# Performance work log

Measured on AMD Instinct MI355X. Metric: run time of the kernel, lower is better.

Reference implementation:

```python
import jax, jax.numpy as jnp
import numpy as np

GROUPS = 8
EPS = 1e-3  # keras GroupNormalization default epsilon


def group_norm(x, gamma, beta):
    # Keras GroupNormalization(axis=-1): reduce over all non-batch, non-group axes.
    B, L, C = x.shape
    xg = x.reshape(B, L, GROUPS, C // GROUPS)
    mean = jnp.mean(xg, axis=(1, 3), keepdims=True)          # [B,1,G,1]
    var = jnp.var(xg, axis=(1, 3), keepdims=True)
    xn = ((xg - mean) * jax.lax.rsqrt(var + EPS)).reshape(B, L, C)
    return xn * gamma + beta


def setup_inputs() -> dict:
    key = jax.random.key(0)
    ks = jax.random.split(key, 6)
    B, L, C = 8, 2048, 512
    x = jax.random.normal(ks[0], (B, L, C), dtype=jnp.float32)
    s = 0.02
    return {
        "x": x,
        "gamma": jnp.ones((C,), jnp.float32),
        "beta": jnp.zeros((C,), jnp.float32),
        "wq": jax.random.normal(ks[1], (C, C), jnp.float32) * s,
        "bq": jnp.zeros((C,), jnp.float32),
        "wk": jax.random.normal(ks[2], (C, C), jnp.float32) * s,
        "bk": jnp.zeros((C,), jnp.float32),
        "wv": jax.random.normal(ks[3], (C, C), jnp.float32) * s,
        "bv": jnp.zeros((C,), jnp.float32),
        "wp": jax.random.normal(ks[4], (C, C), jnp.float32) * s,
        "bp": jnp.zeros((C,), jnp.float32),
    }


def reference(x, gamma, beta, wq, bq, wk, bk, wv, bv, wp, bp):
    C = x.shape[-1]
    scale = jnp.float32(C) ** -0.5
    h = group_norm(x, gamma, beta)                           # normalized input (also residual!)
    q = h @ wq + bq                                          # [B,L,C]
    k = h @ wk + bk
    v = h @ wv + bv
    attn = jnp.einsum('blc,bLc->blL', q, k) * scale          # [B,L,L]
    attn = jax.nn.softmax(attn, axis=-1)
    o = jnp.einsum('blL,bLc->blc', attn, v)                  # [B,L,C]
    o = o @ wp + bp
    return h + o
```

## Files before the change

kernel.cpp:

```cpp
#include <hip/hip_runtime.h>
#include <hip/hip_bf16.h>
#include <cstdint>

typedef unsigned short ushort_t;
typedef __bf16  bf16x8 __attribute__((ext_vector_type(8)));
typedef float   f32x4  __attribute__((ext_vector_type(4)));

#define L_SEQ 2048
#define C_DIM 512
#define B_SZ  8
#define N_GROUPS 8
#define CG 64

__device__ __forceinline__ float bf2f(ushort_t u) {
    union { uint32_t i; float f; } x; x.i = ((uint32_t)u) << 16; return x.f;
}
__device__ __forceinline__ ushort_t f2bf(float f) {
    union { float f; uint32_t i; } x; x.f = f;
    uint32_t i = x.i;
    uint32_t r = (i + 0x7FFFu + ((i >> 16) & 1u)) >> 16;
    return (ushort_t)r;
}

__device__ __forceinline__ void gl_lds16(const ushort_t* g, ushort_t* l) {
    __builtin_amdgcn_global_load_lds(
        (const __attribute__((address_space(1))) unsigned int*)g,
        (__attribute__((address_space(3))) unsigned int*)l, 16, 0, 0);
}

__global__ __launch_bounds__(256) void conv_wT(const float* __restrict__ wq,
                                               const float* __restrict__ wk,
                                               const float* __restrict__ wv,
                                               const float* __restrict__ wp,
                                               ushort_t* __restrict__ wqkvT,
                                               ushort_t* __restrict__ wpT) {
    __shared__ ushort_t Ts[64][72];
    int blk = blockIdx.x, tid = threadIdx.x;
    int mat = blk >> 6, t = blk & 63;
    int k0 = (t >> 3) * 64, n0 = (t & 7) * 64;
    const float* srcs[4] = {wq, wk, wv, wp};
    const float* src = srcs[mat];
    #pragma unroll
    for (int i = 0; i < 2; ++i) {
        int idx = tid * 2 + i;
        int row = idx >> 3, c8 = (idx & 7) * 8;
        const float* p = src + (size_t)(k0 + row) * 512 + n0 + c8;
        float4 a = *(const float4*)p;
        float4 b = *(const float4*)(p + 4);
        Ts[row][c8 + 0] = f2bf(a.x); Ts[row][c8 + 1] = f2bf(a.y);
        Ts[row][c8 + 2] = f2bf(a.z); Ts[row][c8 + 3] = f2bf(a.w);
        Ts[row][c8 + 4] = f2bf(b.x); Ts[row][c8 + 5] = f2bf(b.y);
        Ts[row][c8 + 6] = f2bf(b.z); Ts[row][c8 + 7] = f2bf(b.w);
    }
    __syncthreads();
    int dr = tid >> 2, lc = (tid & 3) * 16;
    union { uint4 v[2]; ushort_t u[16]; } o;
    #pragma unroll
    for (int j = 0; j < 16; ++j) o.u[j] = Ts[lc + j][dr];
    ushort_t* dst = (mat == 3 ? wpT + (size_t)(n0 + dr) * 512
                              : wqkvT + (size_t)(mat * 512 + n0 + dr) * 512) + k0 + lc;
    *(uint4*)dst = o.v[0];
    *(uint4*)(dst + 8) = o.v[1];
}

__global__ __launch_bounds__(256) void gn_stats(const float* __restrict__ x,
                                                float* __restrict__ sums) {
    int bg = blockIdx.x >> 3, sp = blockIdx.x & 7;
    int b = bg >> 3, g = bg & 7;
    int tid = threadIdx.x;
    const float* base = x + ((size_t)b * L_SEQ + sp * 256) * C_DIM + g * CG;
    float s = 0.f, s2 = 0.f;
    #pragma unroll
    for (int it = 0; it < 8; ++it) {
        int i = it * 2048 + tid * 8;
        int l = i >> 6, c = i & 63;
        const float* p = base + (size_t)l * C_DIM + c;
        float4 a = *(const float4*)p;
        float4 bb = *(const float4*)(p + 4);
        s  += a.x + a.y + a.z + a.w + bb.x + bb.y + bb.z + bb.w;
        s2 += a.x*a.x + a.y*a.y + a.z*a.z + a.w*a.w
            + bb.x*bb.x + bb.y*bb.y + bb.z*bb.z + bb.w*bb.w;
    }
    #pragma unroll
    for (int off = 32; off > 0; off >>= 1) { s += __shfl_down(s, off); s2 += __shfl_down(s2, off); }
    __shared__ float rs[4], rs2[4];
    int wave = tid >> 6;
    if ((tid & 63) == 0) { rs[wave] = s; rs2[wave] = s2; }
    __syncthreads();
    if (tid == 0) {
        sums[bg * 16 + sp * 2 + 0] = rs[0] + rs[1] + rs[2] + rs[3];
        sums[bg * 16 + sp * 2 + 1] = rs2[0] + rs2[1] + rs2[2] + rs2[3];
    }
}

__global__ __launch_bounds__(256) void gn_apply(const float* __restrict__ x,
                                                const float* __restrict__ gamma,
                                                const float* __restrict__ beta,
                                                const float* __restrict__ sums,
                                                ushort_t* __restrict__ h) {
    size_t e = ((size_t)blockIdx.x * 256 + threadIdx.x) * 8;
    int c = (int)(e % C_DIM);
    size_t bl = e / C_DIM;
    int b = (int)(bl / L_SEQ);
    int g = c >> 6;
    int bg = b * 8 + g;
    float s = 0.f, s2 = 0.f;
    #pragma unroll
    for (int sp = 0; sp < 8; ++sp) { s += sums[bg * 16 + sp * 2]; s2 += sums[bg * 16 + sp * 2 + 1]; }
    const float N = (float)(L_SEQ * CG);
    float mean = s / N;
    float var  = s2 / N - mean * mean;
    float rstd = rsqrtf(var + 1e-3f);
    float4 a = *(const float4*)(x + e);
    float4 bb = *(const float4*)(x + e + 4);
    float xf[8] = {a.x, a.y, a.z, a.w, bb.x, bb.y, bb.z, bb.w};
    union { uint4 v; ushort_t u[8]; } o;
    #pragma unroll
    for (int i = 0; i < 8; ++i)
        o.u[i] = f2bf((xf[i] - mean) * rstd * gamma[c + i] + beta[c + i]);
    *(uint4*)(h + e) = o.v;
}

template<int MODE>
__global__ __launch_bounds__(256) void gemm128(const ushort_t* __restrict__ A,
                                               const ushort_t* __restrict__ BT,
                                               const float* __restrict__ b0,
                                               const float* __restrict__ b1,
                                               const ushort_t* __restrict__ res,
                                               ushort_t* __restrict__ o0,
                                               ushort_t* __restrict__ o1,
                                               float* __restrict__ of) {
    __shared__ ushort_t As[128][64];
    __shared__ ushort_t Bs[128][64];
    int tid = threadIdx.x, lane = tid & 63, w = tid >> 6;
    int l15 = lane & 15, quad = lane >> 4;
    int m0 = blockIdx.y * 128;
    int n0g = blockIdx.x * 128;
    int wm = w >> 1, wn = w & 1;
    int lr8 = lane >> 3;
    int gch = (lane & 7) ^ lr8;
    int h8  = l15 & 7;
    f32x4 acc[4][4] = {};
    for (int k0 = 0; k0 < 512; k0 += 64) {
        #pragma unroll
        for (int j = 0; j < 4; ++j) {
            int rb = w * 32 + j * 8;
            int r  = rb + lr8;
            gl_lds16(A  + (size_t)(m0 + r) * 512 + k0 + gch * 8, &As[rb][0]);
            gl_lds16(BT + (size_t)(n0g + r) * 512 + k0 + gch * 8, &Bs[rb][0]);
        }
        __syncthreads();
        #pragma unroll
        for (int kk = 0; kk < 2; ++kk) {
            int slot = ((quad + 4 * kk) ^ h8) * 8;
            bf16x8 af[4], bf[4];
            #pragma unroll
            for (int t = 0; t < 4; ++t) {
                af[t] = *(const bf16x8*)&As[wm * 64 + t * 16 + l15][slot];
                bf[t] = *(const bf16x8*)&Bs[wn * 64 + t * 16 + l15][slot];
            }
            #pragma unroll
            for (int mt = 0; mt < 4; ++mt)
                #pragma unroll
                for (int nt = 0; nt < 4; ++nt)
                    acc[mt][nt] = __builtin_amdgcn_mfma_f32_16x16x32_bf16(af[mt], bf[nt], acc[mt][nt], 0, 0, 0);
        }
        __syncthreads();
    }
    #pragma unroll
    for (int mt = 0; mt < 4; ++mt)
        #pragma unroll
        for (int nt = 0; nt < 4; ++nt) {
            int n = (MODE == 0 ? (n0g & 511) : n0g) + wn * 64 + nt * 16 + l15;
            float bvn = (MODE == 2) ? 0.f : (MODE == 1 ? b0[n] : (n0g >> 9 ? b1[n] : b0[n]));
            #pragma unroll
            for (int r = 0; r < 4; ++r) {
                int m = m0 + wm * 64 + mt * 16 + quad * 4 + r;
                float v = acc[mt][nt][r];
                if (MODE == 2) {
                    v += b0[m];
                    o0[(size_t)(n >> 11) * 1048576 + (size_t)m * 2048 + (n & 2047)] = f2bf(v);
                } else if (MODE == 1) {
                    of[(size_t)m * 512 + n] = v + bvn + bf2f(res[(size_t)m * 512 + n]);
                } else {
                    ushort_t* ob = (n0g >> 9) ? o1 : o0;
                    ob[(size_t)m * 512 + n] = f2bf(v + bvn);
                }
            }
        }
}

__global__ __launch_bounds__(768, 3) void attn11(const ushort_t* __restrict__ Q,
                                                 const ushort_t* __restrict__ K,
                                                 const ushort_t* __restrict__ vT,
                                                 ushort_t* __restrict__ O) {
    __shared__ ushort_t Ks[2][32][520];
    __shared__ ushort_t Vs[2][512][32];
    __shared__ ushort_t Ps[2][64][40];
    __shared__ float    Al[2][64];
    __shared__ float    Lb[64];
    int tid = threadIdx.x;
    int lane = tid & 63, w = tid >> 6;
    int l15 = lane & 15, quad = lane >> 4;
    int b  = blockIdx.x & 7;
    int qt = blockIdx.x >> 3;
    const float scale2 = 0.044194173824159216f * 1.4426950408889634f;
    const ushort_t* Qb = Q + (size_t)b * L_SEQ * C_DIM;
    const ushort_t* Kb = K + (size_t)b * L_SEQ * C_DIM;
    const ushort_t* Vt = vT + (size_t)b * C_DIM * L_SEQ;
    ushort_t* Ob = O + (size_t)b * L_SEQ * C_DIM;

    bool isQK = (w < 4);
    int pw = w - 4;
    int d0 = pw * 64;

    bf16x8 qf[16];
    float m_r = -1e30f, l_r = 0.f;
    f32x4 acc[4][4];

    if (isQK) {
        int qr = qt * 64 + w * 16 + l15;
        #pragma unroll
        for (int ks = 0; ks < 16; ++ks)
            qf[ks] = *(const bf16x8*)(Qb + (size_t)qr * C_DIM + ks * 32 + quad * 8);
    } else {
        #pragma unroll
        for (int qi = 0; qi < 4; ++qi)
            #pragma unroll
            for (int nt = 0; nt < 4; ++nt) acc[qi][nt] = (f32x4){0.f, 0.f, 0.f, 0.f};
        #pragma unroll
        for (int i = 0; i < 4; ++i) {
            int row = pw * 4 + i;
            gl_lds16(Kb + (size_t)row * C_DIM + lane * 8, &Ks[0][row][0]);
        }
    }
    __syncthreads();

    for (int kt = 0; kt <= 64; ++kt) {
        int cur = kt & 1, prv = cur ^ 1;
        if (isQK) {
            if (kt < 64) {
                f32x4 s0a = (f32x4){0.f, 0.f, 0.f, 0.f};
                f32x4 s0b = (f32x4){0.f, 0.f, 0.f, 0.f};
                f32x4 s1a = (f32x4){0.f, 0.f, 0.f, 0.f};
                f32x4 s1b = (f32x4){0.f, 0.f, 0.f, 0.f};
                __builtin_amdgcn_s_setprio(1);
                #pragma unroll
                for (int ks = 0; ks < 16; ks += 2) {
                    bf16x8 kf0 = *(const bf16x8*)&Ks[cur][l15][ks * 32 + quad * 8];
                    bf16x8 kf1 = *(const bf16x8*)&Ks[cur][16 + l15][ks * 32 + quad * 8];
                    bf16x8 kf2 = *(const bf16x8*)&Ks[cur][l15][(ks + 1) * 32 + quad * 8];
                    bf16x8 kf3 = *(const bf16x8*)&Ks[cur][16 + l15][(ks + 1) * 32 + quad * 8];
                    s0a = __builtin_amdgcn_mfma_f32_16x16x32_bf16(kf0, qf[ks], s0a, 0, 0, 0);
                    s1a = __builtin_amdgcn_mfma_f32_16x16x32_bf16(kf1, qf[ks], s1a, 0, 0, 0);
                    s0b = __builtin_amdgcn_mfma_f32_16x16x32_bf16(kf2, qf[ks + 1], s0b, 0, 0, 0);
                    s1b = __builtin_amdgcn_mfma_f32_16x16x32_bf16(kf3, qf[ks + 1], s1b, 0, 0, 0);
                }
                __builtin_amdgcn_s_setprio(0);
                f32x4 s0 = s0a + s0b;
                f32x4 s1 = s1a + s1b;
                float mx = fmaxf(fmaxf(fmaxf(s0[0], s0[1]), fmaxf(s0[2], s0[3])),
                                 fmaxf(fmaxf(s1[0], s1[1]), fmaxf(s1[2], s1[3])));
                mx = fmaxf(mx, __shfl_xor(mx, 16, 64));
                mx = fmaxf(mx, __shfl_xor(mx, 32, 64));
                mx *= scale2;
                float mn = fmaxf(m_r, mx);
                float alpha = exp2f(m_r - mn);
                m_r = mn;
                ushort_t pb[8];
                float rs = 0.f;
                #pragma unroll
                for (int r = 0; r < 4; ++r) {
                    pb[r]     = f2bf(exp2f(s0[r] * scale2 - mn));
                    pb[4 + r] = f2bf(exp2f(s1[r] * scale2 - mn));
                    rs += bf2f(pb[r]) + bf2f(pb[4 + r]);
                }
                rs += __shfl_xor(rs, 16, 64);
                rs += __shfl_xor(rs, 32, 64);
                l_r = l_r * alpha + rs;
                int row = w * 16 + l15;
                uint2 w0, w1;
                w0.x = (uint32_t)pb[0] | ((uint32_t)pb[1] << 16);
                w0.y = (uint32_t)pb[2] | ((uint32_t)pb[3] << 16);
                w1.x = (uint32_t)pb[4] | ((uint32_t)pb[5] << 16);
                w1.y = (uint32_t)pb[6] | ((uint32_t)pb[7] << 16);
                *(uint2*)&Ps[cur][row][quad * 4] = w0;
                *(uint2*)&Ps[cur][row][16 + quad * 4] = w1;
                if (lane < 16) Al[cur][w * 16 + lane] = alpha;
            } else {
                if (lane < 16) Lb[w * 16 + lane] = l_r;
            }
        } else {
            if (kt < 63) {
                #pragma unroll
                for (int i = 0; i < 4; ++i) {
                    int row = pw * 4 + i;
                    gl_lds16(Kb + (size_t)((kt + 1) * 32 + row) * C_DIM + lane * 8, &Ks[prv][row][0]);
                }
            }
            if (kt < 64) {
                int k0 = kt * 32;
                #pragma unroll
                for (int i = 0; i < 4; ++i) {
                    int r0 = (pw * 4 + i) * 16;
                    gl_lds16(Vt + (size_t)(r0 + (lane >> 2)) * L_SEQ + k0 + (lane & 3) * 8,
                             &Vs[cur][r0][0]);
                }
            }
            if (kt > 0) {
                bf16x8 pf[4];
                #pragma unroll
                for (int qi = 0; qi < 4; ++qi)
                    pf[qi] = *(const bf16x8*)&Ps[prv][qi * 16 + l15][quad * 8];
                #pragma unroll
                for (int qi = 0; qi < 4; ++qi) {
                    float4 av = *(const float4*)&Al[prv][qi * 16 + quad * 4];
                    #pragma unroll
                    for (int nt = 0; nt < 4; ++nt) {
                        acc[qi][nt][0] *= av.x; acc[qi][nt][1] *= av.y;
                        acc[qi][nt][2] *= av.z; acc[qi][nt][3] *= av.w;
                    }
                }
                bf16x8 vf[4];
                #pragma unroll
                for (int nt = 0; nt < 4; ++nt)
                    vf[nt] = *(const bf16x8*)&Vs[prv][d0 + nt * 16 + l15][quad * 8];
                __builtin_amdgcn_s_setprio(1);
                #pragma unroll
                for (int nt = 0; nt < 4; ++nt)
                    #pragma unroll
                    for (int qi = 0; qi < 4; ++qi)
                        acc[qi][nt] = __builtin_amdgcn_mfma_f32_16x16x32_bf16(pf[qi], vf[nt], acc[qi][nt], 0, 0, 0);
                __builtin_amdgcn_s_setprio(0);
            }
        }
        __syncthreads();
    }
    if (!isQK) {
        #pragma unroll
        for (int qi = 0; qi < 4; ++qi) {
            float4 lv = *(const float4*)&Lb[qi * 16 + quad * 4];
            float inv[4] = {1.f / lv.x, 1.f / lv.y, 1.f / lv.z, 1.f / lv.w};
            #pragma unroll
            for (int r = 0; r < 4; ++r) {
                int m = qt * 64 + qi * 16 + quad * 4 + r;
                #pragma unroll
                for (int nt = 0; nt < 4; ++nt)
                    Ob[(size_t)m * 512 + d0 + nt * 16 + l15] = f2bf(acc[qi][nt][r] * inv[r]);
            }
        }
    }
}

extern "C" void kernel_launch(void* const* d_in, const int* in_sizes, int n_in,
                              void* d_out, int out_size, void* d_ws, size_t ws_size,
                              hipStream_t stream) {
    const float* x     = (const float*)d_in[0];
    const float* gamma = (const float*)d_in[1];
    const float* beta  = (const float*)d_in[2];
    const float* wq    = (const float*)d_in[3];
    const float* bq    = (const float*)d_in[4];
    const float* wk    = (const float*)d_in[5];
    const float* bk    = (const float*)d_in[6];
    const float* wv    = (const float*)d_in[7];
    const float* bv    = (const float*)d_in[8];
    const float* wp    = (const float*)d_in[9];
    const float* bp    = (const float*)d_in[10];
    float* out = (float*)d_out;

    const size_t MC = (size_t)B_SZ * L_SEQ * C_DIM;
    const size_t WC = (size_t)C_DIM * C_DIM;
    ushort_t* h     = (ushort_t*)d_ws;
    ushort_t* qb    = h     + MC;
    ushort_t* kb    = qb    + MC;
    ushort_t* vbuf  = kb    + MC;
    ushort_t* vtb   = vbuf  + MC;
    ushort_t* wqkvT = vtb   + MC;
    ushort_t* wpT   = wqkvT + 3 * WC;
    float* sums     = (float*)(wpT + WC);

    conv_wT<<<dim3(256), dim3(256), 0, stream>>>(wq, wk, wv, wp, wqkvT, wpT);
    gn_stats<<<dim3(512), dim3(256), 0, stream>>>(x, sums);
    gn_apply<<<dim3(4096), dim3(256), 0, stream>>>(x, gamma, beta, sums, h);

    gemm128<0><<<dim3(8, 128), dim3(256), 0, stream>>>(h, wqkvT, bq, bk, nullptr,
                                                       qb, kb, nullptr);
    gemm128<2><<<dim3(128, 4), dim3(256), 0, stream>>>(wqkvT + 2 * WC, h, bv, nullptr, nullptr,
                                                       vtb, nullptr, nullptr);

    attn11<<<dim3(256), dim3(768), 0, stream>>>(qb, kb, vtb, vbuf);

    gemm128<1><<<dim3(4, 128), dim3(256), 0, stream>>>(vbuf, wpT, bp, nullptr, h,
                                                       nullptr, nullptr, out);
}
```

Before: 319.8 us.

## Read V directly from global in attention, merge weight-convert and stats kernels

The PV waves now load V fragments straight from global memory (vT layout) into registers instead of staging them through a double-buffered LDS array. This removes the Vs shared buffer and its async copies. The QK MFMA chain is split into four independent accumulators instead of two to shorten dependency chains. The weight transpose/convert and group-norm stats kernels are fused into one launch to save a kernel launch. The occupancy hint is lowered to 2 blocks per CU, and uncoalesced global V reads on the critical path may add latency.

```diff
diff --git a/kernel.cpp b/kernel.cpp
--- a/kernel.cpp
+++ b/kernel.cpp
@@ -28,68 +28,70 @@
         (__attribute__((address_space(3))) unsigned int*)l, 16, 0, 0);
 }
 
-__global__ __launch_bounds__(256) void conv_wT(const float* __restrict__ wq,
-                                               const float* __restrict__ wk,
-                                               const float* __restrict__ wv,
-                                               const float* __restrict__ wp,
-                                               ushort_t* __restrict__ wqkvT,
-                                               ushort_t* __restrict__ wpT) {
-    __shared__ ushort_t Ts[64][72];
-    int blk = blockIdx.x, tid = threadIdx.x;
-    int mat = blk >> 6, t = blk & 63;
-    int k0 = (t >> 3) * 64, n0 = (t & 7) * 64;
-    const float* srcs[4] = {wq, wk, wv, wp};
-    const float* src = srcs[mat];
-    #pragma unroll
-    for (int i = 0; i < 2; ++i) {
-        int idx = tid * 2 + i;
-        int row = idx >> 3, c8 = (idx & 7) * 8;
-        const float* p = src + (size_t)(k0 + row) * 512 + n0 + c8;
-        float4 a = *(const float4*)p;
-        float4 b = *(const float4*)(p + 4);
-        Ts[row][c8 + 0] = f2bf(a.x); Ts[row][c8 + 1] = f2bf(a.y);
-        Ts[row][c8 + 2] = f2bf(a.z); Ts[row][c8 + 3] = f2bf(a.w);
-        Ts[row][c8 + 4] = f2bf(b.x); Ts[row][c8 + 5] = f2bf(b.y);
-        Ts[row][c8 + 6] = f2bf(b.z); Ts[row][c8 + 7] = f2bf(b.w);
-    }
-    __syncthreads();
-    int dr = tid >> 2, lc = (tid & 3) * 16;
-    union { uint4 v[2]; ushort_t u[16]; } o;
-    #pragma unroll
-    for (int j = 0; j < 16; ++j) o.u[j] = Ts[lc + j][dr];
-    ushort_t* dst = (mat == 3 ? wpT + (size_t)(n0 + dr) * 512
-                              : wqkvT + (size_t)(mat * 512 + n0 + dr) * 512) + k0 + lc;
-    *(uint4*)dst = o.v[0];
-    *(uint4*)(dst + 8) = o.v[1];
-}
-
-__global__ __launch_bounds__(256) void gn_stats(const float* __restrict__ x,
-                                                float* __restrict__ sums) {
-    int bg = blockIdx.x >> 3, sp = blockIdx.x & 7;
-    int b = bg >> 3, g = bg & 7;
+__global__ __launch_bounds__(256) void conv_stats(const float* __restrict__ wq,
+                                                  const float* __restrict__ wk,
+                                                  const float* __restrict__ wv,
+                                                  const float* __restrict__ wp,
+                                                  ushort_t* __restrict__ wqkvT,
+                                                  ushort_t* __restrict__ wpT,
+                                                  const float* __restrict__ x,
+                                                  float* __restrict__ sums) {
     int tid = threadIdx.x;
-    const float* base = x + ((size_t)b * L_SEQ + sp * 256) * C_DIM + g * CG;
-    float s = 0.f, s2 = 0.f;
-    #pragma unroll
-    for (int it = 0; it < 8; ++it) {
-        int i = it * 2048 + tid * 8;
-        int l = i >> 6, c = i & 63;
-        const float* p = base + (size_t)l * C_DIM + c;
-        float4 a = *(const float4*)p;
-        float4 bb = *(const float4*)(p + 4);
-        s  += a.x + a.y + a.z + a.w + bb.x + bb.y + bb.z + bb.w;
-        s2 += a.x*a.x + a.y*a.y + a.z*a.z + a.w*a.w
-            + bb.x*bb.x + bb.y*bb.y + bb.z*bb.z + bb.w*bb.w;
-    }
-    #pragma unroll
-    for (int off = 32; off > 0; off >>= 1) { s += __shfl_down(s, off); s2 += __shfl_down(s2, off); }
-    __shared__ float rs[4], rs2[4];
-    int wave = tid >> 6;
-    if ((tid & 63) == 0) { rs[wave] = s; rs2[wave] = s2; }
-    __syncthreads();
-    if (tid == 0) {
-        sums[bg * 16 + sp * 2 + 0] = rs[0] + rs[1] + rs[2] + rs[3];
-        sums[bg * 16 + sp * 2 + 1] = rs2[0] + rs2[1] + rs2[2] + rs2[3];
+    if (blockIdx.x < 256) {
+        __shared__ ushort_t Ts[64][72];
+        int blk = blockIdx.x;
+        int mat = blk >> 6, t = blk & 63;
+        int k0 = (t >> 3) * 64, n0 = (t & 7) * 64;
+        const float* srcs[4] = {wq, wk, wv, wp};
+        const float* src = srcs[mat];
+        #pragma unroll
+        for (int i = 0; i < 2; ++i) {
+            int idx = tid * 2 + i;
+            int row = idx >> 3, c8 = (idx & 7) * 8;
+            const float* p = src + (size_t)(k0 + row) * 512 + n0 + c8;
+            float4 a = *(const float4*)p;
+            float4 b = *(const float4*)(p + 4);
+            Ts[row][c8 + 0] = f2bf(a.x); Ts[row][c8 + 1] = f2bf(a.y);
+            Ts[row][c8 + 2] = f2bf(a.z); Ts[row][c8 + 3] = f2bf(a.w);
+            Ts[row][c8 + 4] = f2bf(b.x); Ts[row][c8 + 5] = f2bf(b.y);
+            Ts[row][c8 + 6] = f2bf(b.z); Ts[row][c8 + 7] = f2bf(b.w);
+        }
+        __syncthreads();
+        int dr = tid >> 2, lc = (tid & 3) * 16;
+        union { uint4 v[2]; ushort_t u[16]; } o;
+        #pragma unroll
+        for (int j = 0; j < 16; ++j) o.u[j] = Ts[lc + j][dr];
+        ushort_t* dst = (mat == 3 ? wpT + (size_t)(n0 + dr) * 512
+                                  : wqkvT + (size_t)(mat * 512 + n0 + dr) * 512) + k0 + lc;
+        *(uint4*)dst = o.v[0];
+        *(uint4*)(dst + 8) = o.v[1];
+    } else {
+        int bid = blockIdx.x - 256;
+        int bg = bid >> 3, sp = bid & 7;
+        int b = bg >> 3, g = bg & 7;
+        const float* base = x + ((size_t)b * L_SEQ + sp * 256) * C_DIM + g * CG;
+        float s = 0.f, s2 = 0.f;
+        #pragma unroll
+        for (int it = 0; it < 8; ++it) {
+            int i = it * 2048 + tid * 8;
+            int l = i >> 6, c = i & 63;
+            const float* p = base + (size_t)l * C_DIM + c;
+            float4 a = *(const float4*)p;
+            float4 bb = *(const float4*)(p + 4);
+            s  += a.x + a.y + a.z + a.w + bb.x + bb.y + bb.z + bb.w;
+            s2 += a.x*a.x + a.y*a.y + a.z*a.z + a.w*a.w
+                + bb.x*bb.x + bb.y*bb.y + bb.z*bb.z + bb.w*bb.w;
+        }
+        #pragma unroll
+        for (int off = 32; off > 0; off >>= 1) { s += __shfl_down(s, off); s2 += __shfl_down(s2, off); }
+        __shared__ float rs[4], rs2[4];
+        int wave = tid >> 6;
+        if ((tid & 63) == 0) { rs[wave] = s; rs2[wave] = s2; }
+        __syncthreads();
+        if (tid == 0) {
+            sums[bg * 16 + sp * 2 + 0] = rs[0] + rs[1] + rs[2] + rs[3];
+            sums[bg * 16 + sp * 2 + 1] = rs2[0] + rs2[1] + rs2[2] + rs2[3];
+        }
     }
 }
 
@@ -190,12 +192,11 @@
         }
 }
 
-__global__ __launch_bounds__(768, 3) void attn11(const ushort_t* __restrict__ Q,
+__global__ __launch_bounds__(768, 2) void attn12(const ushort_t* __restrict__ Q,
                                                  const ushort_t* __restrict__ K,
                                                  const ushort_t* __restrict__ vT,
                                                  ushort_t* __restrict__ O) {
     __shared__ ushort_t Ks[2][32][520];
-    __shared__ ushort_t Vs[2][512][32];
     __shared__ ushort_t Ps[2][64][40];
     __shared__ float    Al[2][64];
     __shared__ float    Lb[64];
@@ -240,25 +241,26 @@
         int cur = kt & 1, prv = cur ^ 1;
         if (isQK) {
             if (kt < 64) {
-                f32x4 s0a = (f32x4){0.f, 0.f, 0.f, 0.f};
-                f32x4 s0b = (f32x4){0.f, 0.f, 0.f, 0.f};
-                f32x4 s1a = (f32x4){0.f, 0.f, 0.f, 0.f};
-                f32x4 s1b = (f32x4){0.f, 0.f, 0.f, 0.f};
+                f32x4 sa[4], sb[4];
+                #pragma unroll
+                for (int j = 0; j < 4; ++j) {
+                    sa[j] = (f32x4){0.f, 0.f, 0.f, 0.f};
+                    sb[j] = (f32x4){0.f, 0.f, 0.f, 0.f};
+                }
                 __builtin_amdgcn_s_setprio(1);
                 #pragma unroll
-                for (int ks = 0; ks < 16; ks += 2) {
-                    bf16x8 kf0 = *(const bf16x8*)&Ks[cur][l15][ks * 32 + quad * 8];
-                    bf16x8 kf1 = *(const bf16x8*)&Ks[cur][16 + l15][ks * 32 + quad * 8];
-                    bf16x8 kf2 = *(const bf16x8*)&Ks[cur][l15][(ks + 1) * 32 + quad * 8];
-                    bf16x8 kf3 = *(const bf16x8*)&Ks[cur][16 + l15][(ks + 1) * 32 + quad * 8];
-                    s0a = __builtin_amdgcn_mfma_f32_16x16x32_bf16(kf0, qf[ks], s0a, 0, 0, 0);
-                    s1a = __builtin_amdgcn_mfma_f32_16x16x32_bf16(kf1, qf[ks], s1a, 0, 0, 0);
-                    s0b = __builtin_amdgcn_mfma_f32_16x16x32_bf16(kf2, qf[ks + 1], s0b, 0, 0, 0);
-                    s1b = __builtin_amdgcn_mfma_f32_16x16x32_bf16(kf3, qf[ks + 1], s1b, 0, 0, 0);
+                for (int ks = 0; ks < 16; ks += 4) {
+                    #pragma unroll
+                    for (int j = 0; j < 4; ++j) {
+                        bf16x8 kf0 = *(const bf16x8*)&Ks[cur][l15][(ks + j) * 32 + quad * 8];
+                        bf16x8 kf1 = *(const bf16x8*)&Ks[cur][16 + l15][(ks + j) * 32 + quad * 8];
+                        sa[j] = __builtin_amdgcn_mfma_f32_16x16x32_bf16(kf0, qf[ks + j], sa[j], 0, 0, 0);
+                        sb[j] = __builtin_amdgcn_mfma_f32_16x16x32_bf16(kf1, qf[ks + j], sb[j], 0, 0, 0);
+                    }
                 }
                 __builtin_amdgcn_s_setprio(0);
-                f32x4 s0 = s0a + s0b;
-                f32x4 s1 = s1a + s1b;
+                f32x4 s0 = (sa[0] + sa[1]) + (sa[2] + sa[3]);
+                f32x4 s1 = (sb[0] + sb[1]) + (sb[2] + sb[3]);
                 float mx = fmaxf(fmaxf(fmaxf(s0[0], s0[1]), fmaxf(s0[2], s0[3])),
                                  fmaxf(fmaxf(s1[0], s1[1]), fmaxf(s1[2], s1[3])));
                 mx = fmaxf(mx, __shfl_xor(mx, 16, 64));
@@ -298,16 +300,12 @@
                     gl_lds16(Kb + (size_t)((kt + 1) * 32 + row) * C_DIM + lane * 8, &Ks[prv][row][0]);
                 }
             }
-            if (kt < 64) {
-                int k0 = kt * 32;
-                #pragma unroll
-                for (int i = 0; i < 4; ++i) {
-                    int r0 = (pw * 4 + i) * 16;
-                    gl_lds16(Vt + (size_t)(r0 + (lane >> 2)) * L_SEQ + k0 + (lane & 3) * 8,
-                             &Vs[cur][r0][0]);
-                }
-            }
             if (kt > 0) {
+                int k0 = (kt - 1) * 32;
+                bf16x8 vf[4];
+                #pragma unroll
+                for (int nt = 0; nt < 4; ++nt)
+                    vf[nt] = *(const bf16x8*)(Vt + (size_t)(d0 + nt * 16 + l15) * L_SEQ + k0 + quad * 8);
                 bf16x8 pf[4];
                 #pragma unroll
                 for (int qi = 0; qi < 4; ++qi)
@@ -321,10 +319,6 @@
                         acc[qi][nt][2] *= av.z; acc[qi][nt][3] *= av.w;
                     }
                 }
-                bf16x8 vf[4];
-                #pragma unroll
-                for (int nt = 0; nt < 4; ++nt)
-                    vf[nt] = *(const bf16x8*)&Vs[prv][d0 + nt * 16 + l15][quad * 8];
                 __builtin_amdgcn_s_setprio(1);
                 #pragma unroll
                 for (int nt = 0; nt < 4; ++nt)
@@ -379,8 +373,7 @@
     ushort_t* wpT   = wqkvT + 3 * WC;
     float* sums     = (float*)(wpT + WC);
 
-    conv_wT<<<dim3(256), dim3(256), 0, stream>>>(wq, wk, wv, wp, wqkvT, wpT);
-    gn_stats<<<dim3(512), dim3(256), 0, stream>>>(x, sums);
+    conv_stats<<<dim3(768), dim3(256), 0, stream>>>(wq, wk, wv, wp, wqkvT, wpT, x, sums);
     gn_apply<<<dim3(4096), dim3(256), 0, stream>>>(x, gamma, beta, sums, h);
 
     gemm128<0><<<dim3(8, 128), dim3(256), 0, stream>>>(h, wqkvT, bq, bk, nullptr,
@@ -388,7 +381,7 @@
     gemm128<2><<<dim3(128, 4), dim3(256), 0, stream>>>(wqkvT + 2 * WC, h, bv, nullptr, nullptr,
                                                        vtb, nullptr, nullptr);
 
-    attn11<<<dim3(256), dim3(768), 0, stream>>>(qb, kb, vtb, vbuf);
+    attn12<<<dim3(256), dim3(768), 0, stream>>>(qb, kb, vtb, vbuf);
 
     gemm128<1><<<dim3(4, 128), dim3(256), 0, stream>>>(vbuf, wpT, bp, nullptr, h,
                                                        nullptr, nullptr, out);
```

Result: slower. 350.3 us (+9.5%).

## Merge weight-convert with GN stats and QK with V-transpose GEMM launches, swizzle blocks

Applied to the files above, without the earlier changes.

Combines the weight conversion and group-norm statistics kernels into one launch, split by block index. The Q/K GEMM and the transposed-V GEMM also become a single launch of 1536 blocks. Block-index swizzling is added to the QKV and projection GEMMs to improve L2 reuse. The goal is to remove launch overhead and the tail gaps between small kernels, at the cost of branchy kernels with mixed block roles.

```diff
diff --git a/kernel.cpp b/kernel.cpp
--- a/kernel.cpp
+++ b/kernel.cpp
@@ -28,68 +28,70 @@
         (__attribute__((address_space(3))) unsigned int*)l, 16, 0, 0);
 }
 
-__global__ __launch_bounds__(256) void conv_wT(const float* __restrict__ wq,
-                                               const float* __restrict__ wk,
-                                               const float* __restrict__ wv,
-                                               const float* __restrict__ wp,
-                                               ushort_t* __restrict__ wqkvT,
-                                               ushort_t* __restrict__ wpT) {
-    __shared__ ushort_t Ts[64][72];
-    int blk = blockIdx.x, tid = threadIdx.x;
-    int mat = blk >> 6, t = blk & 63;
-    int k0 = (t >> 3) * 64, n0 = (t & 7) * 64;
-    const float* srcs[4] = {wq, wk, wv, wp};
-    const float* src = srcs[mat];
-    #pragma unroll
-    for (int i = 0; i < 2; ++i) {
-        int idx = tid * 2 + i;
-        int row = idx >> 3, c8 = (idx & 7) * 8;
-        const float* p = src + (size_t)(k0 + row) * 512 + n0 + c8;
-        float4 a = *(const float4*)p;
-        float4 b = *(const float4*)(p + 4);
-        Ts[row][c8 + 0] = f2bf(a.x); Ts[row][c8 + 1] = f2bf(a.y);
-        Ts[row][c8 + 2] = f2bf(a.z); Ts[row][c8 + 3] = f2bf(a.w);
-        Ts[row][c8 + 4] = f2bf(b.x); Ts[row][c8 + 5] = f2bf(b.y);
-        Ts[row][c8 + 6] = f2bf(b.z); Ts[row][c8 + 7] = f2bf(b.w);
-    }
-    __syncthreads();
-    int dr = tid >> 2, lc = (tid & 3) * 16;
-    union { uint4 v[2]; ushort_t u[16]; } o;
-    #pragma unroll
-    for (int j = 0; j < 16; ++j) o.u[j] = Ts[lc + j][dr];
-    ushort_t* dst = (mat == 3 ? wpT + (size_t)(n0 + dr) * 512
-                              : wqkvT + (size_t)(mat * 512 + n0 + dr) * 512) + k0 + lc;
-    *(uint4*)dst = o.v[0];
-    *(uint4*)(dst + 8) = o.v[1];
-}
-
-__global__ __launch_bounds__(256) void gn_stats(const float* __restrict__ x,
-                                                float* __restrict__ sums) {
-    int bg = blockIdx.x >> 3, sp = blockIdx.x & 7;
-    int b = bg >> 3, g = bg & 7;
+__global__ __launch_bounds__(256) void conv_stats(const float* __restrict__ wq,
+                                                  const float* __restrict__ wk,
+                                                  const float* __restrict__ wv,
+                                                  const float* __restrict__ wp,
+                                                  ushort_t* __restrict__ wqkvT,
+                                                  ushort_t* __restrict__ wpT,
+                                                  const float* __restrict__ x,
+                                                  float* __restrict__ sums) {
     int tid = threadIdx.x;
-    const float* base = x + ((size_t)b * L_SEQ + sp * 256) * C_DIM + g * CG;
-    float s = 0.f, s2 = 0.f;
-    #pragma unroll
-    for (int it = 0; it < 8; ++it) {
-        int i = it * 2048 + tid * 8;
-        int l = i >> 6, c = i & 63;
-        const float* p = base + (size_t)l * C_DIM + c;
-        float4 a = *(const float4*)p;
-        float4 bb = *(const float4*)(p + 4);
-        s  += a.x + a.y + a.z + a.w + bb.x + bb.y + bb.z + bb.w;
-        s2 += a.x*a.x + a.y*a.y + a.z*a.z + a.w*a.w
-            + bb.x*bb.x + bb.y*bb.y + bb.z*bb.z + bb.w*bb.w;
-    }
-    #pragma unroll
-    for (int off = 32; off > 0; off >>= 1) { s += __shfl_down(s, off); s2 += __shfl_down(s2, off); }
-    __shared__ float rs[4], rs2[4];
-    int wave = tid >> 6;
-    if ((tid & 63) == 0) { rs[wave] = s; rs2[wave] = s2; }
-    __syncthreads();
-    if (tid == 0) {
-        sums[bg * 16 + sp * 2 + 0] = rs[0] + rs[1] + rs[2] + rs[3];
-        sums[bg * 16 + sp * 2 + 1] = rs2[0] + rs2[1] + rs2[2] + rs2[3];
+    if (blockIdx.x < 256) {
+        __shared__ ushort_t Ts[64][72];
+        int blk = blockIdx.x;
+        int mat = blk >> 6, t = blk & 63;
+        int k0 = (t >> 3) * 64, n0 = (t & 7) * 64;
+        const float* srcs[4] = {wq, wk, wv, wp};
+        const float* src = srcs[mat];
+        #pragma unroll
+        for (int i = 0; i < 2; ++i) {
+            int idx = tid * 2 + i;
+            int row = idx >> 3, c8 = (idx & 7) * 8;
+            const float* p = src + (size_t)(k0 + row) * 512 + n0 + c8;
+            float4 a = *(const float4*)p;
+            float4 b = *(const float4*)(p + 4);
+            Ts[row][c8 + 0] = f2bf(a.x); Ts[row][c8 + 1] = f2bf(a.y);
+            Ts[row][c8 + 2] = f2bf(a.z); Ts[row][c8 + 3] = f2bf(a.w);
+            Ts[row][c8 + 4] = f2bf(b.x); Ts[row][c8 + 5] = f2bf(b.y);
+            Ts[row][c8 + 6] = f2bf(b.z); Ts[row][c8 + 7] = f2bf(b.w);
+        }
+        __syncthreads();
+        int dr = tid >> 2, lc = (tid & 3) * 16;
+        union { uint4 v[2]; ushort_t u[16]; } o;
+        #pragma unroll
+        for (int j = 0; j < 16; ++j) o.u[j] = Ts[lc + j][dr];
+        ushort_t* dst = (mat == 3 ? wpT + (size_t)(n0 + dr) * 512
+                                  : wqkvT + (size_t)(mat * 512 + n0 + dr) * 512) + k0 + lc;
+        *(uint4*)dst = o.v[0];
+        *(uint4*)(dst + 8) = o.v[1];
+    } else {
+        int bid = blockIdx.x - 256;
+        int bg = bid >> 3, sp = bid & 7;
+        int b = bg >> 3, g = bg & 7;
+        const float* base = x + ((size_t)b * L_SEQ + sp * 256) * C_DIM + g * CG;
+        float s = 0.f, s2 = 0.f;
+        #pragma unroll
+        for (int it = 0; it < 8; ++it) {
+            int i = it * 2048 + tid * 8;
+            int l = i >> 6, c = i & 63;
+            const float* p = base + (size_t)l * C_DIM + c;
+            float4 a = *(const float4*)p;
+            float4 bb = *(const float4*)(p + 4);
+            s  += a.x + a.y + a.z + a.w + bb.x + bb.y + bb.z + bb.w;
+            s2 += a.x*a.x + a.y*a.y + a.z*a.z + a.w*a.w
+                + bb.x*bb.x + bb.y*bb.y + bb.z*bb.z + bb.w*bb.w;
+        }
+        #pragma unroll
+        for (int off = 32; off > 0; off >>= 1) { s += __shfl_down(s, off); s2 += __shfl_down(s2, off); }
+        __shared__ float rs[4], rs2[4];
+        int wave = tid >> 6;
+        if ((tid & 63) == 0) { rs[wave] = s; rs2[wave] = s2; }
+        __syncthreads();
+        if (tid == 0) {
+            sums[bg * 16 + sp * 2 + 0] = rs[0] + rs[1] + rs[2] + rs[3];
+            sums[bg * 16 + sp * 2 + 1] = rs2[0] + rs2[1] + rs2[2] + rs2[3];
+        }
     }
 }
 
@@ -121,21 +123,33 @@
     *(uint4*)(h + e) = o.v;
 }
 
-template<int MODE>
-__global__ __launch_bounds__(256) void gemm128(const ushort_t* __restrict__ A,
-                                               const ushort_t* __restrict__ BT,
-                                               const float* __restrict__ b0,
-                                               const float* __restrict__ b1,
-                                               const ushort_t* __restrict__ res,
-                                               ushort_t* __restrict__ o0,
-                                               ushort_t* __restrict__ o1,
-                                               float* __restrict__ of) {
+__global__ __launch_bounds__(256) void gemm_qkv(const ushort_t* __restrict__ h,
+                                                const ushort_t* __restrict__ wqkvT,
+                                                const float* __restrict__ bq,
+                                                const float* __restrict__ bk,
+                                                const float* __restrict__ bv,
+                                                ushort_t* __restrict__ qb,
+                                                ushort_t* __restrict__ kb,
+                                                ushort_t* __restrict__ vtb) {
     __shared__ ushort_t As[128][64];
     __shared__ ushort_t Bs[128][64];
+    int id = blockIdx.x;
+    const ushort_t *A, *BT;
+    int m0, n0g, vmode;
+    if (id < 1024) {
+        int swz = (id & 7) * 128 + (id >> 3);
+        n0g = (swz & 7) * 128;
+        m0  = (swz >> 3) * 128;
+        A = h; BT = wqkvT; vmode = 0;
+    } else {
+        int vid = id - 1024;
+        int swz = (vid & 7) * 64 + (vid >> 3);
+        n0g = (swz >> 2) * 128;
+        m0  = (swz & 3) * 128;
+        A = wqkvT + 2 * (size_t)C_DIM * C_DIM; BT = h; vmode = 1;
+    }
     int tid = threadIdx.x, lane = tid & 63, w = tid >> 6;
     int l15 = lane & 15, quad = lane >> 4;
-    int m0 = blockIdx.y * 128;
-    int n0g = blockIdx.x * 128;
     int wm = w >> 1, wn = w & 1;
     int lr8 = lane >> 3;
     int gch = (lane & 7) ^ lr8;
@@ -167,25 +181,93 @@
         }
         __syncthreads();
     }
+    if (vmode == 0) {
+        int seg = n0g >> 9;
+        const float* bias = seg ? bk : bq;
+        ushort_t* ob = seg ? kb : qb;
+        int ns = n0g & 511;
+        #pragma unroll
+        for (int mt = 0; mt < 4; ++mt)
+            #pragma unroll
+            for (int nt = 0; nt < 4; ++nt) {
+                int n = ns + wn * 64 + nt * 16 + l15;
+                float bvn = bias[n];
+                #pragma unroll
+                for (int r = 0; r < 4; ++r) {
+                    int m = m0 + wm * 64 + mt * 16 + quad * 4 + r;
+                    ob[(size_t)m * 512 + n] = f2bf(acc[mt][nt][r] + bvn);
+                }
+            }
+    } else {
+        #pragma unroll
+        for (int mt = 0; mt < 4; ++mt)
+            #pragma unroll
+            for (int nt = 0; nt < 4; ++nt) {
+                int n = n0g + wn * 64 + nt * 16 + l15;
+                #pragma unroll
+                for (int r = 0; r < 4; ++r) {
+                    int m = m0 + wm * 64 + mt * 16 + quad * 4 + r;
+                    float v = acc[mt][nt][r] + bv[m];
+                    vtb[(size_t)(n >> 11) * 1048576 + (size_t)m * 2048 + (n & 2047)] = f2bf(v);
+                }
+            }
+    }
+}
+
+__global__ __launch_bounds__(256) void gemm_proj(const ushort_t* __restrict__ A,
+                                                 const ushort_t* __restrict__ BT,
+                                                 const float* __restrict__ b0,
+                                                 const ushort_t* __restrict__ res,
+                                                 float* __restrict__ of) {
+    __shared__ ushort_t As[128][64];
+    __shared__ ushort_t Bs[128][64];
+    int id = blockIdx.x;
+    int swz = (id & 7) * 64 + (id >> 3);
+    int n0g = (swz & 3) * 128;
+    int m0  = (swz >> 2) * 128;
+    int tid = threadIdx.x, lane = tid & 63, w = tid >> 6;
+    int l15 = lane & 15, quad = lane >> 4;
+    int wm = w >> 1, wn = w & 1;
+    int lr8 = lane >> 3;
+    int gch = (lane & 7) ^ lr8;
+    int h8  = l15 & 7;
+    f32x4 acc[4][4] = {};
+    for (int k0 = 0; k0 < 512; k0 += 64) {
+        #pragma unroll
+        for (int j = 0; j < 4; ++j) {
+            int rb = w * 32 + j * 8;
+            int r  = rb + lr8;
+            gl_lds16(A  + (size_t)(m0 + r) * 512 + k0 + gch * 8, &As[rb][0]);
+            gl_lds16(BT + (size_t)(n0g + r) * 512 + k0 + gch * 8, &Bs[rb][0]);
+        }
+        __syncthreads();
+        #pragma unroll
+        for (int kk = 0; kk < 2; ++kk) {
+            int slot = ((quad + 4 * kk) ^ h8) * 8;
+            bf16x8 af[4], bf[4];
+            #pragma unroll
+            for (int t = 0; t < 4; ++t) {
+                af[t] = *(const bf16x8*)&As[wm * 64 + t * 16 + l15][slot];
+                bf[t] = *(const bf16x8*)&Bs[wn * 64 + t * 16 + l15][slot];
+            }
+            #pragma unroll
+            for (int mt = 0; mt < 4; ++mt)
+                #pragma unroll
+                for (int nt = 0; nt < 4; ++nt)
+                    acc[mt][nt] = __builtin_amdgcn_mfma_f32_16x16x32_bf16(af[mt], bf[nt], acc[mt][nt], 0, 0, 0);
+        }
+        __syncthreads();
+    }
     #pragma unroll
     for (int mt = 0; mt < 4; ++mt)
         #pragma unroll
         for (int nt = 0; nt < 4; ++nt) {
-            int n = (MODE == 0 ? (n0g & 511) : n0g) + wn * 64 + nt * 16 + l15;
-            float bvn = (MODE == 2) ? 0.f : (MODE == 1 ? b0[n] : (n0g >> 9 ? b1[n] : b0[n]));
+            int n = n0g + wn * 64 + nt * 16 + l15;
+            float bvn = b0[n];
             #pragma unroll
             for (int r = 0; r < 4; ++r) {
                 int m = m0 + wm * 64 + mt * 16 + quad * 4 + r;
-                float v = acc[mt][nt][r];
-                if (MODE == 2) {
-                    v += b0[m];
-                    o0[(size_t)(n >> 11) * 1048576 + (size_t)m * 2048 + (n & 2047)] = f2bf(v);
-                } else if (MODE == 1) {
-                    of[(size_t)m * 512 + n] = v + bvn + bf2f(res[(size_t)m * 512 + n]);
-                } else {
-                    ushort_t* ob = (n0g >> 9) ? o1 : o0;
-                    ob[(size_t)m * 512 + n] = f2bf(v + bvn);
-                }
+                of[(size_t)m * 512 + n] = acc[mt][nt][r] + bvn + bf2f(res[(size_t)m * 512 + n]);
             }
         }
 }
@@ -379,17 +461,12 @@
     ushort_t* wpT   = wqkvT + 3 * WC;
     float* sums     = (float*)(wpT + WC);
 
-    conv_wT<<<dim3(256), dim3(256), 0, stream>>>(wq, wk, wv, wp, wqkvT, wpT);
-    gn_stats<<<dim3(512), dim3(256), 0, stream>>>(x, sums);
+    conv_stats<<<dim3(768), dim3(256), 0, stream>>>(wq, wk, wv, wp, wqkvT, wpT, x, sums);
     gn_apply<<<dim3(4096), dim3(256), 0, stream>>>(x, gamma, beta, sums, h);
 
-    gemm128<0><<<dim3(8, 128), dim3(256), 0, stream>>>(h, wqkvT, bq, bk, nullptr,
-                                                       qb, kb, nullptr);
-    gemm128<2><<<dim3(128, 4), dim3(256), 0, stream>>>(wqkvT + 2 * WC, h, bv, nullptr, nullptr,
-                                                       vtb, nullptr, nullptr);
+    gemm_qkv<<<dim3(1536), dim3(256), 0, stream>>>(h, wqkvT, bq, bk, bv, qb, kb, vtb);
 
     attn11<<<dim3(256), dim3(768), 0, stream>>>(qb, kb, vtb, vbuf);
 
-    gemm128<1><<<dim3(4, 128), dim3(256), 0, stream>>>(vbuf, wpT, bp, nullptr, h,
-                                                       nullptr, nullptr, out);
-}
+    gemm_proj<<<dim3(512), dim3(256), 0, stream>>>(vbuf, wpT, bp, h, out);
+}
```

Result: faster. 307.7 us (median of 2 runs) (-3.8%).
